# Kernel tuning notes

Hardware: AMD Instinct MI355X
Metric: run time of the kernel (lower is better)

The kernel has to match this reference:

```python
import jax, jax.numpy as jnp
import numpy as np
from jax import lax

SIM_THRESH = 0.9
MOTION_SCALE = 0.5
SALIENCY_SCALE = 0.5
EPS = 1e-6


def setup_inputs() -> dict:
    key = jax.random.key(0)
    k1, k2, k3, k4 = jax.random.split(key, 4)
    B, N, D, H, W = 128, 196, 768, 14, 14
    return {
        "tokens": jax.random.normal(k1, (B, N, D), dtype=jnp.float32),
        "motion_magnitude": jax.random.uniform(k2, (B, 1, H, W), dtype=jnp.float32),
        "saliency_map": jax.random.uniform(k3, (B, 1, H, W), dtype=jnp.float32),
        "compression_ratio": jax.random.uniform(k4, (B, H, W), dtype=jnp.float32),
    }


def _importance(motion, saliency, ratio):
    # motion/saliency are already (B,1,14,14) == (height,width), so
    # adaptive_avg_pool2d to (14,14) is the identity.
    B = motion.shape[0]
    m = motion.reshape(B, -1)
    m = m / (jnp.max(m) + EPS)               # global max, as in torch .max()
    s = saliency.reshape(B, -1)
    s = s / (jnp.max(s) + EPS)
    r = ratio.reshape(B, -1)
    imp = (MOTION_SCALE * m + SALIENCY_SCALE * s
           + (1.0 - MOTION_SCALE - SALIENCY_SCALE) * r)
    lo = imp.min(axis=1, keepdims=True)
    hi = imp.max(axis=1, keepdims=True)
    return (imp - lo) / (hi - lo + EPS)      # (B, N)


def _groups(adj):
    """Sequential BFS grouping over roots, faithful to the torch loop.

    adj: bool (N,N) directed edge mask. Returns (group_ids int32 (N,), num_groups).
    """
    N = adj.shape[0]

    def root_step(carry, r):
        assigned, gids, gid = carry

        def assign(c):
            assigned, gids, gid = c
            # BFS from root r, only through currently-unassigned nodes
            allowed = (~assigned).at[r].set(True)
            reach0 = jnp.zeros(N, dtype=bool).at[r].set(True)

            def body(s):
                reach, _ = s
                nxt = reach | (jnp.any(adj & reach[:, None], axis=0) & allowed)
                return nxt, jnp.any(nxt != reach)

            reach, _ = lax.while_loop(lambda s: s[1], body, (reach0, True))
            return assigned | reach, jnp.where(reach, gid, gids), gid + 1

        carry = lax.cond(assigned[r], lambda c: c, assign, carry)
        return carry, None

    init = (jnp.zeros(N, dtype=bool), jnp.zeros(N, dtype=jnp.int32), jnp.int32(0))
    (_, gids, ngroups), _ = lax.scan(root_step, init, jnp.arange(N))
    return gids, ngroups


def _merge_one(tokens_b, imp_b, adj_b):
    N = tokens_b.shape[0]
    gids, ng = _groups(adj_b)
    denom = jax.ops.segment_sum(imp_b, gids, num_segments=N) + EPS
    w = imp_b / denom[gids]
    merged = jax.ops.segment_sum(tokens_b * w[:, None], gids, num_segments=N)
    return merged, gids, ng


def reference(tokens, motion_magnitude, saliency_map, compression_ratio):
    B, N, D = tokens.shape
    imp = _importance(motion_magnitude, saliency_map, compression_ratio)  # (B,N)

    # cosine similarity (F.normalize with eps=1e-12)
    norm = jnp.maximum(jnp.linalg.norm(tokens, axis=-1, keepdims=True), 1e-12)
    tn = tokens / norm
    sim = jnp.einsum('bnd,bmd->bnm', tn, tn)
    sim = sim * (1.0 - jnp.eye(N, dtype=sim.dtype))  # zero diagonal

    # directed merge mask: similarity * (1 - importance_row)
    mask = (sim > SIM_THRESH).astype(sim.dtype) * (1.0 - imp[:, :, None])
    adj = mask > 0.5

    merged, gids, ng = jax.vmap(_merge_one)(tokens, imp, adj)
    # merged padded to N groups (rows >= num_groups are zero)
    return merged, sim, imp, gids
```

## Files before the change

### kernel.cpp

```cpp
#include <hip/hip_runtime.h>
#include <cstdint>

static constexpr int cB = 128;
static constexpr int cN = 196;
static constexpr int cD = 768;
static constexpr int cNN = cN * cN;
static constexpr int cND = cN * cD;
static constexpr float cEPS = 1e-6f;
static constexpr size_t cBND = (size_t)cB * cN * cD;

typedef __attribute__((ext_vector_type(8))) short short8;
typedef __attribute__((ext_vector_type(8))) unsigned short u16x8;
typedef __attribute__((ext_vector_type(4))) float f32x4;
typedef unsigned long long u64;

__device__ __forceinline__ unsigned short bf16_rne(float x) {
    unsigned u = __builtin_bit_cast(unsigned, x);
    u += 0x7FFFu + ((u >> 16) & 1u);
    return (unsigned short)(u >> 16);
}

__global__ __launch_bounds__(256) void k_imp(const float* __restrict__ mo,
                                             const float* __restrict__ sa,
                                             float* __restrict__ out_imp,
                                             float* __restrict__ ws_imp,
                                             float* __restrict__ ws_w,
                                             u64* __restrict__ ws_adj) {
    int b = blockIdx.x, t = threadIdx.x;
    __shared__ float redm[4], reds[4], lo_s[4], hi_s[4], MS[2], LOHI[2];

    for (int i = b * 256 + t; i < cB * cN * 4; i += cB * 256) ws_adj[i] = 0ull;

    const float4* mo4 = (const float4*)mo;
    const float4* sa4 = (const float4*)sa;
    float mm = 0.f, ms = 0.f;
    for (int i = t; i < cB * cN / 4; i += 256) {
        float4 a = mo4[i], c = sa4[i];
        mm = fmaxf(mm, fmaxf(fmaxf(a.x, a.y), fmaxf(a.z, a.w)));
        ms = fmaxf(ms, fmaxf(fmaxf(c.x, c.y), fmaxf(c.z, c.w)));
    }
    #pragma unroll
    for (int off = 32; off; off >>= 1) {
        mm = fmaxf(mm, __shfl_down(mm, off));
        ms = fmaxf(ms, __shfl_down(ms, off));
    }
    if ((t & 63) == 0) { redm[t >> 6] = mm; reds[t >> 6] = ms; }
    __syncthreads();
    if (t == 0) {
        float a = redm[0], c = reds[0];
        for (int w = 1; w < 4; w++) { a = fmaxf(a, redm[w]); c = fmaxf(c, reds[w]); }
        MS[0] = 1.0f / (a + cEPS);
        MS[1] = 1.0f / (c + cEPS);
    }
    __syncthreads();
    float Minv = MS[0], Sinv = MS[1];
    float v = 0.f, lo = 1e30f, hi = -1e30f;
    if (t < cN) {
        v = 0.5f * mo[b * cN + t] * Minv + 0.5f * sa[b * cN + t] * Sinv;
        lo = v; hi = v;
    }
    #pragma unroll
    for (int off = 32; off; off >>= 1) {
        lo = fminf(lo, __shfl_down(lo, off));
        hi = fmaxf(hi, __shfl_down(hi, off));
    }
    if ((t & 63) == 0) { lo_s[t >> 6] = lo; hi_s[t >> 6] = hi; }
    __syncthreads();
    if (t == 0) {
        float l = lo_s[0], h = hi_s[0];
        for (int w = 1; w < 4; w++) { l = fminf(l, lo_s[w]); h = fmaxf(h, hi_s[w]); }
        LOHI[0] = l; LOHI[1] = h;
    }
    __syncthreads();
    if (t < cN) {
        float imp = (v - LOHI[0]) / (LOHI[1] - LOHI[0] + cEPS);
        out_imp[b * cN + t] = imp;
        ws_imp[b * cN + t] = imp;
        ws_w[b * cN + t] = imp / (imp + cEPS);
    }
}

__global__ __launch_bounds__(256, 2) void k_sim(const float* __restrict__ tok,
                                                const float* __restrict__ ws_w,
                                                const float* __restrict__ ws_imp,
                                                float* __restrict__ out_sim,
                                                u64* __restrict__ ws_adj,
                                                float* __restrict__ merged) {
    __shared__ unsigned short sA[128 * 40];
    __shared__ unsigned short sB[128 * 40];
    __shared__ float invR[128], invC[128], impR[128], impC[128];
    __shared__ u64 ldsAdj[256];
    __shared__ u64 ldsAdjT[256];

    int bid = blockIdx.x;
    int xcd = bid & 7;
    int lin = bid >> 3;
    int b   = xcd + 8 * (lin / 3);
    int tc  = lin % 3;
    int rb = (tc == 2) ? 128 : 0;
    int cb = (tc == 0) ? 0 : 128;
    bool diag = (tc != 1);

    int t = threadIdx.x;
    int w = t >> 6, lane = t & 63;
    int lr = lane & 15, kf = (lane >> 4) * 8;
    int wr = (w >> 1) * 64, wc = (w & 1) * 64;
    const size_t bN = (size_t)b * cN;
    const float* tb = tok + bN * cD;
    float* mg = merged + bN * cD;

    ldsAdj[t] = 0ull;
    ldsAdjT[t] = 0ull;
    if (t < 128) {
        int gr = rb + t;
        impR[t] = (gr < cN) ? ws_imp[bN + gr] : 1.f;
    } else {
        int gc = cb + (t - 128);
        impC[t - 128] = (gc < cN) ? ws_imp[bN + gc] : 1.f;
    }

    f32x4 acc[4][4];
    #pragma unroll
    for (int i = 0; i < 4; i++)
        #pragma unroll
        for (int j = 0; j < 4; j++) acc[i][j] = (f32x4){0.f, 0.f, 0.f, 0.f};

    int srow = t >> 2;
    int q = t & 3;

    float wA0 = 0.f, wA1 = 0.f;
    if (diag) {
        int g0 = rb + srow, g1 = rb + srow + 64;
        if (g0 < cN) wA0 = ws_w[bN + g0];
        if (g1 < cN) wA1 = ws_w[bN + g1];
    }
    float sa0 = 0.f, sa1 = 0.f, sb0 = 0.f, sb1 = 0.f;

    float4 bufA[8], bufB[8];

    auto LOADS = [&](int k0, float4 (&r)[8]) {
        int koff = k0 + 8 * q;
        #pragma unroll
        for (int p = 0; p < 2; ++p) {
            int row = srow + 64 * p;
            float4 z = make_float4(0.f, 0.f, 0.f, 0.f);
            r[2 * p] = z; r[2 * p + 1] = z;
            int gr = rb + row;
            if (gr < cN) {
                const float4* pa = (const float4*)(tb + (size_t)gr * cD + koff);
                r[2 * p] = pa[0]; r[2 * p + 1] = pa[1];
            }
            if (!diag) {
                r[4 + 2 * p] = z; r[4 + 2 * p + 1] = z;
                int gc = cb + row;
                if (gc < cN) {
                    const float4* pb = (const float4*)(tb + (size_t)gc * cD + koff);
                    r[4 + 2 * p] = pb[0]; r[4 + 2 * p + 1] = pb[1];
                }
            }
        }
    };
    auto PACK = [&](const float4 (&r)[8], int k0p) {
        int koff = k0p + 8 * q;
        #pragma unroll
        for (int p = 0; p < 2; ++p) {
            int row = srow + 64 * p;
            float4 a0 = r[2 * p], a1 = r[2 * p + 1];
            float ds = a0.x * a0.x + a0.y * a0.y + a0.z * a0.z + a0.w * a0.w
                     + a1.x * a1.x + a1.y * a1.y + a1.z * a1.z + a1.w * a1.w;
            if (p) sa1 += ds; else sa0 += ds;
            u16x8 ha;
            ha[0] = bf16_rne(a0.x); ha[1] = bf16_rne(a0.y);
            ha[2] = bf16_rne(a0.z); ha[3] = bf16_rne(a0.w);
            ha[4] = bf16_rne(a1.x); ha[5] = bf16_rne(a1.y);
            ha[6] = bf16_rne(a1.z); ha[7] = bf16_rne(a1.w);
            *(u16x8*)&sA[row * 40 + 8 * q] = ha;
            if (diag) {
                int gr = rb + row;
                if (gr < cN) {
                    float wv = p ? wA1 : wA0;
                    float4* md = (float4*)(mg + (size_t)gr * cD + koff);
                    md[0] = make_float4(a0.x * wv, a0.y * wv, a0.z * wv, a0.w * wv);
                    md[1] = make_float4(a1.x * wv, a1.y * wv, a1.z * wv, a1.w * wv);
                }
            } else {
                float4 b0 = r[4 + 2 * p], b1 = r[4 + 2 * p + 1];
                float dsb = b0.x * b0.x + b0.y * b0.y + b0.z * b0.z + b0.w * b0.w
                          + b1.x * b1.x + b1.y * b1.y + b1.z * b1.z + b1.w * b1.w;
                if (p) sb1 += dsb; else sb0 += dsb;
                u16x8 hb;
                hb[0] = bf16_rne(b0.x); hb[1] = bf16_rne(b0.y);
                hb[2] = bf16_rne(b0.z); hb[3] = bf16_rne(b0.w);
                hb[4] = bf16_rne(b1.x); hb[5] = bf16_rne(b1.y);
                hb[6] = bf16_rne(b1.z); hb[7] = bf16_rne(b1.w);
                *(u16x8*)&sB[row * 40 + 8 * q] = hb;
            }
        }
    };
    auto COMPUTE = [&]() {
        short8 af[4], bf[4];
        #pragma unroll
        for (int rg = 0; rg < 4; rg++)
            af[rg] = *(const short8*)&sA[(wr + 16 * rg + lr) * 40 + kf];
        const unsigned short* sS = diag ? sA : sB;
        #pragma unroll
        for (int cg = 0; cg < 4; cg++)
            bf[cg] = *(const short8*)&sS[(wc + 16 * cg + lr) * 40 + kf];
        #pragma unroll
        for (int rg = 0; rg < 4; rg++)
            #pragma unroll
            for (int cg = 0; cg < 4; cg++)
                acc[rg][cg] = __builtin_amdgcn_mfma_f32_16x16x32_bf16(
                    af[rg], bf[cg], acc[rg][cg], 0, 0, 0);
    };

    LOADS(0, bufA);
    for (int k0 = 0; k0 < cD; k0 += 64) {
        PACK(bufA, k0);
        __syncthreads();
        LOADS(k0 + 32, bufB);
        COMPUTE();
        __syncthreads();

        PACK(bufB, k0 + 32);
        __syncthreads();
        if (k0 + 64 < cD) LOADS(k0 + 64, bufA);
        COMPUTE();
        __syncthreads();
    }

    sa0 += __shfl_xor(sa0, 1); sa0 += __shfl_xor(sa0, 2);
    sa1 += __shfl_xor(sa1, 1); sa1 += __shfl_xor(sa1, 2);
    if (!diag) {
        sb0 += __shfl_xor(sb0, 1); sb0 += __shfl_xor(sb0, 2);
        sb1 += __shfl_xor(sb1, 1); sb1 += __shfl_xor(sb1, 2);
    }
    if (q == 0) {
        invR[srow] = sa0; invR[srow + 64] = sa1;
        if (diag) { invC[srow] = sa0; invC[srow + 64] = sa1; }
        else      { invC[srow] = sb0; invC[srow + 64] = sb1; }
    }
    __syncthreads();
    if (t < 128) invR[t] = 1.0f / fmaxf(sqrtf(invR[t]), 1e-12f);
    else { int c = t - 128; invC[c] = 1.0f / fmaxf(sqrtf(invC[c]), 1e-12f); }
    __syncthreads();

    float* so = out_sim + (size_t)b * cNN;
    int wloc = w >> 1;
    #pragma unroll
    for (int rg = 0; rg < 4; rg++) {
        int rBaseLoc = wr + 16 * rg + (lane >> 4) * 4;
        #pragma unroll
        for (int cg = 0; cg < 4; cg++) {
            int cLoc = wc + 16 * cg + lr;
            int C = cb + cLoc;
            if (C >= cN) continue;
            float ic = invC[cLoc];
            float imC = impC[cLoc];
            u64 bits = 0ull;
            #pragma unroll
            for (int i = 0; i < 4; i++) {
                int rLoc = rBaseLoc + i;
                int R = rb + rLoc;
                if (R >= cN) continue;
                float val = (R == C) ? 0.f : acc[rg][cg][i] * invR[rLoc] * ic;
                so[(size_t)R * cN + C] = val;
                if (val > 0.9f && impR[rLoc] < 0.5f) bits |= 1ull << (R & 63);
                if (!diag) {
                    so[(size_t)C * cN + R] = val;
                    if (val > 0.9f && imC < 0.5f)
                        atomicOr(&ldsAdjT[rLoc * 2 + ((C >> 6) & 1)],
                                 1ull << (C & 63));
                }
            }
            if (bits) atomicOr(&ldsAdj[cLoc * 2 + wloc], bits);
        }
    }
    __syncthreads();
    {
        int cLoc = t >> 1, wl = t & 1;
        int C = cb + cLoc;
        u64 v = ldsAdj[t];
        if (C < cN && v)
            atomicOr(&ws_adj[((size_t)b * cN + C) * 4 + (rb >> 6) + wl], v);
        if (!diag) {
            u64 vt = ldsAdjT[t];
            if (vt)
                atomicOr(&ws_adj[((size_t)b * cN + cLoc) * 4 + 2 + wl], vt);
        }
    }
}

__global__ __launch_bounds__(256) void k_group(const u64* __restrict__ ws_adj,
                                               const float* __restrict__ ws_imp,
                                               const float* __restrict__ tok,
                                               float* __restrict__ out_gids,
                                               float* __restrict__ ws_w,
                                               int* __restrict__ ws_flag,
                                               int* __restrict__ ws_gids,
                                               float* __restrict__ merged) {
    int b = blockIdx.x, t = threadIdx.x;
    __shared__ float impL[cN];
    __shared__ u64 reachw[4], assignedw[4], edge_s[4];
    __shared__ int flag;
    __shared__ int gidsL[cN];
    __shared__ float denomL[cN];
    __shared__ float wL[cN];

    u64 m0 = 0, m1 = 0, m2 = 0, m3 = 0;
    if (t < cN) {
        impL[t] = ws_imp[b * cN + t];
        const u64* ap = ws_adj + ((size_t)b * cN + t) * 4;
        m0 = ap[0]; m1 = ap[1]; m2 = ap[2]; m3 = ap[3];
    }
    u64 anym = m0 | m1 | m2 | m3;
    u64 bal = __ballot(anym != 0ull);
    if ((t & 63) == 0) edge_s[t >> 6] = bal;
    __syncthreads();
    bool has_edges = (edge_s[0] | edge_s[1] | edge_s[2] | edge_s[3]) != 0ull;

    if (!has_edges) {
        if (t < cN) {
            float imp = impL[t];
            ws_w[b * cN + t] = imp / (imp + cEPS);
            ws_gids[b * cN + t] = t;
            out_gids[b * cN + t] = (float)t;
        }
        if (t == 0) ws_flag[b] = 1;
        return;
    }

    if (t < 4) assignedw[t] = 0ull;
    if (t < cN) { gidsL[t] = 0; denomL[t] = 0.f; }
    __syncthreads();
    int gid = 0;
    int wrd_t = t >> 6, bit_t = t & 63;
    for (int r = 0; r < cN; r++) {
        if ((assignedw[r >> 6] >> (r & 63)) & 1ull) continue;
        if (t < 4) reachw[t] = (t == (r >> 6)) ? (1ull << (r & 63)) : 0ull;
        __syncthreads();
        int changed = 1;
        while (changed) {
            u64 hit = (m0 & reachw[0]) | (m1 & reachw[1]) |
                      (m2 & reachw[2]) | (m3 & reachw[3]);
            bool inre = (t < cN) && ((reachw[wrd_t] >> bit_t) & 1ull);
            bool unass = (t < cN) && !((assignedw[wrd_t] >> bit_t) & 1ull);
            bool p = inre || (hit != 0ull && unass);
            u64 nw = __ballot(p);
            __syncthreads();
            if (t == 0) flag = 0;
            __syncthreads();
            if ((t & 63) == 0) {
                if (nw != reachw[t >> 6]) flag = 1;
                reachw[t >> 6] = nw;
            }
            __syncthreads();
            changed = flag;
        }
        if ((t < cN) && ((reachw[wrd_t] >> bit_t) & 1ull)) gidsL[t] = gid;
        if (t < 4) assignedw[t] |= reachw[t];
        gid++;
        __syncthreads();
    }
    if (t < cN) atomicAdd(&denomL[gidsL[t]], impL[t]);
    __syncthreads();
    if (t < cN) {
        int g = gidsL[t];
        float wv = impL[t] / (denomL[g] + cEPS);
        ws_w[b * cN + t] = wv;
        wL[t] = wv;
        ws_gids[b * cN + t] = g;
        out_gids[b * cN + t] = (float)g;
    }
    if (t == 0) ws_flag[b] = 0;
    __syncthreads();

    if (t < 192) {
        for (int n = 0; n < cN; n++) {
            float4 acc = make_float4(0.f, 0.f, 0.f, 0.f);
            for (int j = 0; j < cN; j++) {
                if (gidsL[j] == n) {
                    const float4 v = *(const float4*)(tok + (size_t)b * cND + (size_t)j * cD + 4 * t);
                    float wv = wL[j];
                    acc.x += v.x * wv; acc.y += v.y * wv;
                    acc.z += v.z * wv; acc.w += v.w * wv;
                }
            }
            *(float4*)(merged + (size_t)b * cND + (size_t)n * cD + 4 * t) = acc;
        }
    }
}

extern "C" void kernel_launch(void* const* d_in, const int* in_sizes, int n_in,
                              void* d_out, int out_size, void* d_ws, size_t ws_size,
                              hipStream_t stream) {
    const float* tok = (const float*)d_in[0];
    const float* mo  = (const float*)d_in[1];
    const float* sa  = (const float*)d_in[2];

    float* out = (float*)d_out;
    float* out_merged = out;
    float* out_sim    = out + cBND;
    float* out_imp    = out_sim + (size_t)cB * cNN;
    float* out_gids   = out_imp + (size_t)cB * cN;

    u64*   ws_adj  = (u64*)d_ws;
    float* ws_imp  = (float*)(ws_adj + (size_t)cB * cN * 4);
    float* ws_w    = ws_imp + cB * cN;
    int*   ws_flag = (int*)(ws_w + cB * cN);
    int*   ws_gids = ws_flag + cB;

    k_imp<<<cB, 256, 0, stream>>>(mo, sa, out_imp, ws_imp, ws_w, ws_adj);
    k_sim<<<384, 256, 0, stream>>>(tok, ws_w, ws_imp, out_sim, ws_adj, out_merged);
    k_group<<<cB, 256, 0, stream>>>(ws_adj, ws_imp, tok, out_gids, ws_w,
                                    ws_flag, ws_gids, out_merged);
}
```

Measured before the change: 198.3 us.

## Split similarity GEMM into 64x64 upper-triangular tiles for more blocks

Breaks each batch's 196x196 similarity computation from three 128x128 tiles into ten 64x64 upper-triangular tiles, raising the grid from 384 to 1280 blocks with smaller per-block register and LDS footprints and a higher occupancy hint. This targets poor GPU fill and load imbalance, since 384 blocks only lightly cover the CUs. The cost is that each token row is re-read from global memory by more tiles, and each tile does fewer MFMAs per unit of loaded data.

```diff
diff --git a/kernel.cpp b/kernel.cpp
--- a/kernel.cpp
+++ b/kernel.cpp
@@ -80,136 +80,127 @@
     }
 }
 
-__global__ __launch_bounds__(256, 2) void k_sim(const float* __restrict__ tok,
+__global__ __launch_bounds__(256, 5) void k_sim(const float* __restrict__ tok,
                                                 const float* __restrict__ ws_w,
                                                 const float* __restrict__ ws_imp,
                                                 float* __restrict__ out_sim,
                                                 u64* __restrict__ ws_adj,
                                                 float* __restrict__ merged) {
-    __shared__ unsigned short sA[128 * 40];
-    __shared__ unsigned short sB[128 * 40];
-    __shared__ float invR[128], invC[128], impR[128], impC[128];
-    __shared__ u64 ldsAdj[256];
-    __shared__ u64 ldsAdjT[256];
+    __shared__ unsigned short sA[64 * 40];
+    __shared__ unsigned short sB[64 * 40];
+    __shared__ float invR[64], invC[64], impR[64], impC[64];
+    __shared__ u64 ldsAdj[64];
+    __shared__ u64 ldsAdjT[64];
 
     int bid = blockIdx.x;
     int xcd = bid & 7;
     int lin = bid >> 3;
-    int b   = xcd + 8 * (lin / 3);
-    int tc  = lin % 3;
-    int rb = (tc == 2) ? 128 : 0;
-    int cb = (tc == 0) ? 0 : 128;
-    bool diag = (tc != 1);
+    int b   = xcd + 8 * (lin / 10);
+    int tc  = lin % 10;
+    int ri, ci;
+    if      (tc < 4) { ri = 0; ci = tc; }
+    else if (tc < 7) { ri = 1; ci = tc - 3; }
+    else if (tc < 9) { ri = 2; ci = tc - 5; }
+    else             { ri = 3; ci = 3; }
+    int rb = ri * 64, cb = ci * 64;
+    bool diag = (rb == cb);
 
     int t = threadIdx.x;
     int w = t >> 6, lane = t & 63;
     int lr = lane & 15, kf = (lane >> 4) * 8;
-    int wr = (w >> 1) * 64, wc = (w & 1) * 64;
+    int wr = (w >> 1) * 32, wc = (w & 1) * 32;
     const size_t bN = (size_t)b * cN;
     const float* tb = tok + bN * cD;
     float* mg = merged + bN * cD;
 
-    ldsAdj[t] = 0ull;
-    ldsAdjT[t] = 0ull;
-    if (t < 128) {
+    if (t < 64) { ldsAdj[t] = 0ull; ldsAdjT[t] = 0ull; }
+    if (t < 64) {
         int gr = rb + t;
         impR[t] = (gr < cN) ? ws_imp[bN + gr] : 1.f;
-    } else {
-        int gc = cb + (t - 128);
-        impC[t - 128] = (gc < cN) ? ws_imp[bN + gc] : 1.f;
-    }
-
-    f32x4 acc[4][4];
+    } else if (t < 128) {
+        int gc = cb + (t - 64);
+        impC[t - 64] = (gc < cN) ? ws_imp[bN + gc] : 1.f;
+    }
+
+    f32x4 acc[2][2];
     #pragma unroll
-    for (int i = 0; i < 4; i++)
+    for (int i = 0; i < 2; i++)
         #pragma unroll
-        for (int j = 0; j < 4; j++) acc[i][j] = (f32x4){0.f, 0.f, 0.f, 0.f};
+        for (int j = 0; j < 2; j++) acc[i][j] = (f32x4){0.f, 0.f, 0.f, 0.f};
 
     int srow = t >> 2;
     int q = t & 3;
 
-    float wA0 = 0.f, wA1 = 0.f;
+    float wA = 0.f;
     if (diag) {
-        int g0 = rb + srow, g1 = rb + srow + 64;
-        if (g0 < cN) wA0 = ws_w[bN + g0];
-        if (g1 < cN) wA1 = ws_w[bN + g1];
-    }
-    float sa0 = 0.f, sa1 = 0.f, sb0 = 0.f, sb1 = 0.f;
-
-    float4 bufA[8], bufB[8];
-
-    auto LOADS = [&](int k0, float4 (&r)[8]) {
+        int g0 = rb + srow;
+        if (g0 < cN) wA = ws_w[bN + g0];
+    }
+    float sa0 = 0.f, sb0 = 0.f;
+
+    float4 bufA[4], bufB[4];
+
+    auto LOADS = [&](int k0, float4 (&r)[4]) {
         int koff = k0 + 8 * q;
-        #pragma unroll
-        for (int p = 0; p < 2; ++p) {
-            int row = srow + 64 * p;
-            float4 z = make_float4(0.f, 0.f, 0.f, 0.f);
-            r[2 * p] = z; r[2 * p + 1] = z;
-            int gr = rb + row;
+        float4 z = make_float4(0.f, 0.f, 0.f, 0.f);
+        r[0] = z; r[1] = z;
+        int gr = rb + srow;
+        if (gr < cN) {
+            const float4* pa = (const float4*)(tb + (size_t)gr * cD + koff);
+            r[0] = pa[0]; r[1] = pa[1];
+        }
+        if (!diag) {
+            r[2] = z; r[3] = z;
+            int gc = cb + srow;
+            if (gc < cN) {
+                const float4* pb = (const float4*)(tb + (size_t)gc * cD + koff);
+                r[2] = pb[0]; r[3] = pb[1];
+            }
+        }
+    };
+    auto PACK = [&](const float4 (&r)[4], int k0p) {
+        int koff = k0p + 8 * q;
+        float4 a0 = r[0], a1 = r[1];
+        sa0 += a0.x * a0.x + a0.y * a0.y + a0.z * a0.z + a0.w * a0.w
+             + a1.x * a1.x + a1.y * a1.y + a1.z * a1.z + a1.w * a1.w;
+        u16x8 ha;
+        ha[0] = bf16_rne(a0.x); ha[1] = bf16_rne(a0.y);
+        ha[2] = bf16_rne(a0.z); ha[3] = bf16_rne(a0.w);
+        ha[4] = bf16_rne(a1.x); ha[5] = bf16_rne(a1.y);
+        ha[6] = bf16_rne(a1.z); ha[7] = bf16_rne(a1.w);
+        *(u16x8*)&sA[srow * 40 + 8 * q] = ha;
+        if (diag) {
+            int gr = rb + srow;
             if (gr < cN) {
-                const float4* pa = (const float4*)(tb + (size_t)gr * cD + koff);
-                r[2 * p] = pa[0]; r[2 * p + 1] = pa[1];
+                float4* md = (float4*)(mg + (size_t)gr * cD + koff);
+                md[0] = make_float4(a0.x * wA, a0.y * wA, a0.z * wA, a0.w * wA);
+                md[1] = make_float4(a1.x * wA, a1.y * wA, a1.z * wA, a1.w * wA);
             }
-            if (!diag) {
-                r[4 + 2 * p] = z; r[4 + 2 * p + 1] = z;
-                int gc = cb + row;
-                if (gc < cN) {
-                    const float4* pb = (const float4*)(tb + (size_t)gc * cD + koff);
-                    r[4 + 2 * p] = pb[0]; r[4 + 2 * p + 1] = pb[1];
-                }
-            }
-        }
-    };
-    auto PACK = [&](const float4 (&r)[8], int k0p) {
-        int koff = k0p + 8 * q;
-        #pragma unroll
-        for (int p = 0; p < 2; ++p) {
-            int row = srow + 64 * p;
-            float4 a0 = r[2 * p], a1 = r[2 * p + 1];
-            float ds = a0.x * a0.x + a0.y * a0.y + a0.z * a0.z + a0.w * a0.w
-                     + a1.x * a1.x + a1.y * a1.y + a1.z * a1.z + a1.w * a1.w;
-            if (p) sa1 += ds; else sa0 += ds;
-            u16x8 ha;
-            ha[0] = bf16_rne(a0.x); ha[1] = bf16_rne(a0.y);
-            ha[2] = bf16_rne(a0.z); ha[3] = bf16_rne(a0.w);
-            ha[4] = bf16_rne(a1.x); ha[5] = bf16_rne(a1.y);
-            ha[6] = bf16_rne(a1.z); ha[7] = bf16_rne(a1.w);
-            *(u16x8*)&sA[row * 40 + 8 * q] = ha;
-            if (diag) {
-                int gr = rb + row;
-                if (gr < cN) {
-                    float wv = p ? wA1 : wA0;
-                    float4* md = (float4*)(mg + (size_t)gr * cD + koff);
-                    md[0] = make_float4(a0.x * wv, a0.y * wv, a0.z * wv, a0.w * wv);
-                    md[1] = make_float4(a1.x * wv, a1.y * wv, a1.z * wv, a1.w * wv);
-                }
-            } else {
-                float4 b0 = r[4 + 2 * p], b1 = r[4 + 2 * p + 1];
-                float dsb = b0.x * b0.x + b0.y * b0.y + b0.z * b0.z + b0.w * b0.w
-                          + b1.x * b1.x + b1.y * b1.y + b1.z * b1.z + b1.w * b1.w;
-                if (p) sb1 += dsb; else sb0 += dsb;
-                u16x8 hb;
-                hb[0] = bf16_rne(b0.x); hb[1] = bf16_rne(b0.y);
-                hb[2] = bf16_rne(b0.z); hb[3] = bf16_rne(b0.w);
-                hb[4] = bf16_rne(b1.x); hb[5] = bf16_rne(b1.y);
-                hb[6] = bf16_rne(b1.z); hb[7] = bf16_rne(b1.w);
-                *(u16x8*)&sB[row * 40 + 8 * q] = hb;
-            }
+        } else {
+            float4 b0 = r[2], b1 = r[3];
+            sb0 += b0.x * b0.x + b0.y * b0.y + b0.z * b0.z + b0.w * b0.w
+                 + b1.x * b1.x + b1.y * b1.y + b1.z * b1.z + b1.w * b1.w;
+            u16x8 hb;
+            hb[0] = bf16_rne(b0.x); hb[1] = bf16_rne(b0.y);
+            hb[2] = bf16_rne(b0.z); hb[3] = bf16_rne(b0.w);
+            hb[4] = bf16_rne(b1.x); hb[5] = bf16_rne(b1.y);
+            hb[6] = bf16_rne(b1.z); hb[7] = bf16_rne(b1.w);
+            *(u16x8*)&sB[srow * 40 + 8 * q] = hb;
         }
     };
     auto COMPUTE = [&]() {
-        short8 af[4], bf[4];
+        short8 af[2], bf[2];
         #pragma unroll
-        for (int rg = 0; rg < 4; rg++)
+        for (int rg = 0; rg < 2; rg++)
             af[rg] = *(const short8*)&sA[(wr + 16 * rg + lr) * 40 + kf];
         const unsigned short* sS = diag ? sA : sB;
         #pragma unroll
-        for (int cg = 0; cg < 4; cg++)
+        for (int cg = 0; cg < 2; cg++)
             bf[cg] = *(const short8*)&sS[(wc + 16 * cg + lr) * 40 + kf];
         #pragma unroll
-        for (int rg = 0; rg < 4; rg++)
+        for (int rg = 0; rg < 2; rg++)
             #pragma unroll
-            for (int cg = 0; cg < 4; cg++)
+            for (int cg = 0; cg < 2; cg++)
                 acc[rg][cg] = __builtin_amdgcn_mfma_f32_16x16x32_bf16(
                     af[rg], bf[cg], acc[rg][cg], 0, 0, 0);
     };
@@ -230,28 +221,22 @@
     }
 
     sa0 += __shfl_xor(sa0, 1); sa0 += __shfl_xor(sa0, 2);
-    sa1 += __shfl_xor(sa1, 1); sa1 += __shfl_xor(sa1, 2);
-    if (!diag) {
-        sb0 += __shfl_xor(sb0, 1); sb0 += __shfl_xor(sb0, 2);
-        sb1 += __shfl_xor(sb1, 1); sb1 += __shfl_xor(sb1, 2);
-    }
+    if (!diag) { sb0 += __shfl_xor(sb0, 1); sb0 += __shfl_xor(sb0, 2); }
     if (q == 0) {
-        invR[srow] = sa0; invR[srow + 64] = sa1;
-        if (diag) { invC[srow] = sa0; invC[srow + 64] = sa1; }
-        else      { invC[srow] = sb0; invC[srow + 64] = sb1; }
-    }
-    __syncthreads();
-    if (t < 128) invR[t] = 1.0f / fmaxf(sqrtf(invR[t]), 1e-12f);
-    else { int c = t - 128; invC[c] = 1.0f / fmaxf(sqrtf(invC[c]), 1e-12f); }
+        invR[srow] = sa0;
+        invC[srow] = diag ? sa0 : sb0;
+    }
+    __syncthreads();
+    if (t < 64) invR[t] = 1.0f / fmaxf(sqrtf(invR[t]), 1e-12f);
+    else if (t < 128) { int c = t - 64; invC[c] = 1.0f / fmaxf(sqrtf(invC[c]), 1e-12f); }
     __syncthreads();
 
     float* so = out_sim + (size_t)b * cNN;
-    int wloc = w >> 1;
     #pragma unroll
-    for (int rg = 0; rg < 4; rg++) {
+    for (int rg = 0; rg < 2; rg++) {
         int rBaseLoc = wr + 16 * rg + (lane >> 4) * 4;
         #pragma unroll
-        for (int cg = 0; cg < 4; cg++) {
+        for (int cg = 0; cg < 2; cg++) {
             int cLoc = wc + 16 * cg + lr;
             int C = cb + cLoc;
             if (C >= cN) continue;
@@ -269,25 +254,23 @@
                 if (!diag) {
                     so[(size_t)C * cN + R] = val;
                     if (val > 0.9f && imC < 0.5f)
-                        atomicOr(&ldsAdjT[rLoc * 2 + ((C >> 6) & 1)],
-                                 1ull << (C & 63));
+                        atomicOr(&ldsAdjT[rLoc], 1ull << (C & 63));
                 }
             }
-            if (bits) atomicOr(&ldsAdj[cLoc * 2 + wloc], bits);
-        }
-    }
-    __syncthreads();
-    {
-        int cLoc = t >> 1, wl = t & 1;
-        int C = cb + cLoc;
+            if (bits) atomicOr(&ldsAdj[cLoc], bits);
+        }
+    }
+    __syncthreads();
+    if (t < 64) {
+        int C = cb + t;
         u64 v = ldsAdj[t];
         if (C < cN && v)
-            atomicOr(&ws_adj[((size_t)b * cN + C) * 4 + (rb >> 6) + wl], v);
-        if (!diag) {
-            u64 vt = ldsAdjT[t];
-            if (vt)
-                atomicOr(&ws_adj[((size_t)b * cN + cLoc) * 4 + 2 + wl], vt);
-        }
+            atomicOr(&ws_adj[(bN + C) * 4 + (rb >> 6)], v);
+    } else if (t < 128 && !diag) {
+        int R = rb + (t - 64);
+        u64 vt = ldsAdjT[t - 64];
+        if (R < cN && vt)
+            atomicOr(&ws_adj[(bN + R) * 4 + (cb >> 6)], vt);
     }
 }
 
@@ -411,7 +394,7 @@
     int*   ws_gids = ws_flag + cB;
 
     k_imp<<<cB, 256, 0, stream>>>(mo, sa, out_imp, ws_imp, ws_w, ws_adj);
-    k_sim<<<384, 256, 0, stream>>>(tok, ws_w, ws_imp, out_sim, ws_adj, out_merged);
+    k_sim<<<1280, 256, 0, stream>>>(tok, ws_w, ws_imp, out_sim, ws_adj, out_merged);
     k_group<<<cB, 256, 0, stream>>>(ws_adj, ws_imp, tok, out_gids, ws_w,
                                     ws_flag, ws_gids, out_merged);
 }
```

New measurement: 197.4 us. Within noise of the previous version (-0.5%).
